# Kernel tuning notes

Hardware: AMD Instinct MI355X
Metric: run time of the kernel (lower is better)

Reference implementation:

```python
import jax, jax.numpy as jnp
import numpy as np

T = 32400   # bs*H*W BEV queries (1*180*180)
S = 16896   # bs*num_cams*h*w image keys (1*6*32*88)
E = 256     # embed_dim
H = 8       # num_heads
D = 32      # head_dim
MAXL = 32   # max interval length (ref_num_f)


def _mlp(x, w1, b1, w2, b2):
    # nn.Sequential(Linear(E,2E), ReLU, Linear(2E,E))
    return jax.nn.relu(x @ w1 + b1) @ w2 + b2


def setup_inputs() -> dict:
    k0 = jax.random.key(0)
    ks = jax.random.split(k0, 8)
    # ragged interval structure: every BEV cell has an interval of length (idx%32)+1
    lengths = (np.arange(T) % MAXL) + 1
    starts = np.concatenate([np.zeros(1, np.int64), np.cumsum(lengths)[:-1]])
    N = int(lengths.sum())  # 534472 frustum points
    ranks_bev = np.repeat(np.arange(T), lengths)          # sorted by BEV cell
    rng = np.random.default_rng(0)
    ranks_feat = rng.integers(0, S, size=N)               # which key/value row each point reads

    def lin(k, fi, fo):
        return jax.random.normal(k, (fi, fo), jnp.float32) * (1.0 / np.sqrt(fi))

    key_feat = jax.random.normal(ks[1], (S, E), jnp.float32)
    return dict(
        query_depth=jax.random.normal(ks[0], (T, E), jnp.float32),
        key=key_feat,
        value=key_feat,  # module asserts torch.equal(key, value)
        q_w1=lin(ks[2], E, 2 * E), q_b1=jnp.zeros((2 * E,), jnp.float32),
        q_w2=lin(ks[3], 2 * E, E), q_b2=jnp.zeros((E,), jnp.float32),
        k_w1=lin(ks[4], E, 2 * E), k_b1=jnp.zeros((2 * E,), jnp.float32),
        k_w2=lin(ks[5], 2 * E, E), k_b2=jnp.zeros((E,), jnp.float32),
        ranks_feat_f=jnp.asarray(ranks_feat, jnp.int32),
        ranks_bev_f=jnp.asarray(ranks_bev, jnp.int32),
        interval_starts_f=jnp.asarray(starts, jnp.int32),
        interval_lengths_f=jnp.asarray(lengths, jnp.int32),
        ref_num=MAXL,
    )


def reference(query_depth, key, value,
              q_w1, q_b1, q_w2, q_b2,
              k_w1, k_b1, k_w2, k_b2,
              ranks_feat_f, ranks_bev_f,
              interval_starts_f, interval_lengths_f, ref_num):
    scaling = 1.0 / jnp.sqrt(jnp.float32(D))
    q = (_mlp(query_depth, q_w1, q_b1, q_w2, q_b2) * scaling).reshape(T, H, D)
    k = _mlp(key, k_w1, k_b1, k_w2, k_b2).reshape(S, H, D)
    v = value.reshape(S, H, D)

    N = ranks_bev_f.shape[0]
    pt = jnp.arange(N, dtype=jnp.int32)
    # interval id of each point (intervals are contiguous, sorted by start)
    iid = jnp.searchsorted(interval_starts_f, pt, side='right') - 1
    ranks_ref = pt - interval_starts_f[iid]  # within-interval slot, in [0, ref_num)

    # per-point raw attention logit: q[bev] . k[feat] per head  -> [N, H]
    w = jnp.einsum('nhd,nhd->nh', q[ranks_bev_f], k[ranks_feat_f])

    # scatter into ragged weight tensor [T, H, ref_num]; padding masked to -1e9
    attn = jnp.full((T, H, ref_num), -1e9, jnp.float32)
    attn = attn.at[ranks_bev_f, :, ranks_ref].set(w)
    attn = jax.nn.softmax(attn, axis=-1)

    # gather normalized weights back per point and scatter-combine values
    wp = attn[ranks_bev_f, :, ranks_ref]          # [N, H]
    vp = v[ranks_feat_f]                          # [N, H, D]
    out = jnp.zeros((T, H, D), jnp.float32).at[ranks_bev_f].add(wp[:, :, None] * vp)
    return out.reshape(T, E)
```

## Files before the change

kernel.cpp:

```cpp
#include <hip/hip_runtime.h>
#include <hip/hip_bf16.h>
#include <cstdint>
#include <cstddef>

constexpr int T_Q   = 32400;
constexpr int T_PAD = 32512;
constexpr int S_K   = 16896;
constexpr int E_DIM = 256;
constexpr int HID   = 512;

typedef __bf16 bf16x8 __attribute__((ext_vector_type(8)));
typedef float  f32x4  __attribute__((ext_vector_type(4)));

__device__ __forceinline__ void async16(const __hip_bfloat16* gp, __hip_bfloat16* lp) {
    __builtin_amdgcn_global_load_lds(
        (const __attribute__((address_space(1))) void*)(gp),
        (__attribute__((address_space(3))) void*)(lp), 16, 0, 0);
}

__device__ __forceinline__ float b2f(unsigned short u) {
    return __uint_as_float(((unsigned)u) << 16);
}

constexpr int NB_Q = (T_PAD * E_DIM / 4) / 256;
constexpr int NB_K = (S_K * E_DIM / 4) / 256;
constexpr int NB_PREP = NB_Q + NB_K + NB_K + 128;

__global__ __launch_bounds__(256) void prep(
    const float* __restrict__ q_in, const float* __restrict__ key_in,
    const float* __restrict__ val_in,
    const float* __restrict__ s0, const float* __restrict__ s1,
    const float* __restrict__ s2, const float* __restrict__ s3,
    __hip_bfloat16* __restrict__ qA, __hip_bfloat16* __restrict__ kA,
    __hip_bfloat16* __restrict__ vB,
    __hip_bfloat16* __restrict__ d0, __hip_bfloat16* __restrict__ d1,
    __hip_bfloat16* __restrict__ d2, __hip_bfloat16* __restrict__ d3) {
    __shared__ float tb[64][65];
    const int b = blockIdx.x;
    const int tid = threadIdx.x;

    if (b < NB_Q + 2 * NB_K) {
        const float* src;
        __hip_bfloat16* dst;
        int bl, valid;
        if (b < NB_Q) { src = q_in; dst = qA; bl = b; valid = T_Q * E_DIM; }
        else if (b < NB_Q + NB_K) { src = key_in; dst = kA; bl = b - NB_Q; valid = S_K * E_DIM; }
        else { src = val_in; dst = vB; bl = b - NB_Q - NB_K; valid = S_K * E_DIM; }
        int i = (bl * 256 + tid) * 4;
        float4 f = make_float4(0.f, 0.f, 0.f, 0.f);
        if (i < valid) f = *(const float4*)(src + i);
        union { ushort4 u4; __hip_bfloat16 bb[4]; } cv;
        cv.bb[0] = __float2bfloat16(f.x);
        cv.bb[1] = __float2bfloat16(f.y);
        cv.bb[2] = __float2bfloat16(f.z);
        cv.bb[3] = __float2bfloat16(f.w);
        *(ushort4*)(dst + i) = cv.u4;
        return;
    }

    int tloc = b - (NB_Q + 2 * NB_K);
    int m = tloc >> 5;
    int tt = tloc & 31;
    const float* S = m == 0 ? s0 : m == 1 ? s1 : m == 2 ? s2 : s3;
    __hip_bfloat16* D = m == 0 ? d0 : m == 1 ? d1 : m == 2 ? d2 : d3;
    int Kd, Nd, kt, nt;
    if ((m & 1) == 0) { Kd = 256; Nd = 512; kt = tt & 3; nt = tt >> 2; }
    else              { Kd = 512; Nd = 256; kt = tt & 7; nt = tt >> 3; }
    int tx = tid & 63, ty = tid >> 6;
#pragma unroll
    for (int p = 0; p < 16; ++p) {
        int row = ty * 16 + p;
        tb[row][tx] = S[(size_t)(kt * 64 + row) * Nd + nt * 64 + tx];
    }
    __syncthreads();
#pragma unroll
    for (int p = 0; p < 16; ++p) {
        int row = ty * 16 + p;
        D[(size_t)(nt * 64 + row) * Kd + kt * 64 + tx] = __float2bfloat16(tb[tx][row]);
    }
}

constexpr int BM = 128, BN = 128, BK = 32;

__global__ __launch_bounds__(256) void gemm_bf16(
    const __hip_bfloat16* __restrict__ A,
    const __hip_bfloat16* __restrict__ BT,
    const float* __restrict__ bias,
    __hip_bfloat16* __restrict__ C,
    int K, int N, int relu, float scale) {
    __shared__ __hip_bfloat16 As[BM * BK];
    __shared__ __hip_bfloat16 Bs[BN * BK];

    const int ntiles = N >> 7;
    const int tm = blockIdx.x / ntiles;
    const int tn = blockIdx.x - tm * ntiles;
    const size_t m0 = (size_t)tm * BM;
    const int n0 = tn * BN;

    const int tid = threadIdx.x;
    const int w = tid >> 6, l = tid & 63;
    const int lm = l & 15, lq = l >> 4;
    const int wm = (w >> 1) << 6, wn = (w & 1) << 6;

    const int srow = l >> 2;
    const int scol = (((l & 3) ^ (srow & 3)) << 3);

    f32x4 acc[4][4] = {};

    for (int k0 = 0; k0 < K; k0 += BK) {
#pragma unroll
        for (int c = 0; c < 2; ++c) {
            int r = c * 64 + w * 16 + srow;
            async16(A  + (m0 + r) * K + k0 + scol, As + (c * 64 + w * 16) * BK);
            async16(BT + (size_t)(n0 + r) * K + k0 + scol, Bs + (c * 64 + w * 16) * BK);
        }
        __syncthreads();

        const int rsw = ((lq ^ (lm & 3)) << 3);
        bf16x8 af[4], bfr[4];
#pragma unroll
        for (int mi = 0; mi < 4; ++mi)
            af[mi] = *(const bf16x8*)(As + (wm + mi * 16 + lm) * BK + rsw);
#pragma unroll
        for (int ni = 0; ni < 4; ++ni)
            bfr[ni] = *(const bf16x8*)(Bs + (wn + ni * 16 + lm) * BK + rsw);
#pragma unroll
        for (int mi = 0; mi < 4; ++mi)
#pragma unroll
            for (int ni = 0; ni < 4; ++ni)
                acc[mi][ni] = __builtin_amdgcn_mfma_f32_16x16x32_bf16(
                    af[mi], bfr[ni], acc[mi][ni], 0, 0, 0);
        __syncthreads();
    }

#pragma unroll
    for (int ni = 0; ni < 4; ++ni) {
        int col = n0 + wn + ni * 16 + lm;
        float bv = bias[col];
#pragma unroll
        for (int mi = 0; mi < 4; ++mi) {
            size_t rowb = m0 + wm + mi * 16 + lq * 4;
#pragma unroll
            for (int r = 0; r < 4; ++r) {
                float vv = acc[mi][ni][r] + bv;
                if (relu) vv = fmaxf(vv, 0.f);
                C[(rowb + r) * N + col] = __float2bfloat16(vv * scale);
            }
        }
    }
}

#define PREF(K0,K1,K2,K3,V0,V1,V2,V3,J0)                                    \
    {                                                                        \
        int j_ = (J0);                                                       \
        int i0 = su + j_ + 0; i0 = i0 < nmax ? i0 : nmax;                    \
        int i1 = su + j_ + 1; i1 = i1 < nmax ? i1 : nmax;                    \
        int i2 = su + j_ + 2; i2 = i2 < nmax ? i2 : nmax;                    \
        int i3 = su + j_ + 3; i3 = i3 < nmax ? i3 : nmax;                    \
        int f0 = rf[i0], f1 = rf[i1], f2 = rf[i2], f3 = rf[i3];              \
        K0 = *(const ushort4*)(kp + (size_t)f0 * 256 + l4);                  \
        V0 = *(const ushort4*)(vp + (size_t)f0 * 256 + l4);                  \
        K1 = *(const ushort4*)(kp + (size_t)f1 * 256 + l4);                  \
        V1 = *(const ushort4*)(vp + (size_t)f1 * 256 + l4);                  \
        K2 = *(const ushort4*)(kp + (size_t)f2 * 256 + l4);                  \
        V2 = *(const ushort4*)(vp + (size_t)f2 * 256 + l4);                  \
        K3 = *(const ushort4*)(kp + (size_t)f3 * 256 + l4);                  \
        V3 = *(const ushort4*)(vp + (size_t)f3 * 256 + l4);                  \
    }

#define DOT4(K_) fmaf(q0, b2f(K_.x), fmaf(q1, b2f(K_.y), fmaf(q2, b2f(K_.z), q3 * b2f(K_.w))))

#define PROC(K0,K1,K2,K3,V0,V1,V2,V3,J0)                                    \
    {                                                                        \
        float w0 = DOT4(K0), w1 = DOT4(K1), w2 = DOT4(K2), w3 = DOT4(K3);   \
        w0 += __shfl_xor(w0, 1); w1 += __shfl_xor(w1, 1);                   \
        w2 += __shfl_xor(w2, 1); w3 += __shfl_xor(w3, 1);                   \
        w0 += __shfl_xor(w0, 2); w1 += __shfl_xor(w1, 2);                   \
        w2 += __shfl_xor(w2, 2); w3 += __shfl_xor(w3, 2);                   \
        w0 += __shfl_xor(w0, 4); w1 += __shfl_xor(w1, 4);                   \
        w2 += __shfl_xor(w2, 4); w3 += __shfl_xor(w3, 4);                   \
        if ((J0) + 1 >= L) w1 = -1e30f;                                      \
        if ((J0) + 2 >= L) w2 = -1e30f;                                      \
        if ((J0) + 3 >= L) w3 = -1e30f;                                      \
        float mw = fmaxf(fmaxf(w0, w1), fmaxf(w2, w3));                      \
        float mn = fmaxf(m, mw);                                             \
        float al = __expf(m - mn); m = mn;                                   \
        float p0 = __expf(w0 - mn), p1 = __expf(w1 - mn);                    \
        float p2 = __expf(w2 - mn), p3 = __expf(w3 - mn);                    \
        s = s * al + ((p0 + p1) + (p2 + p3));                                \
        a0 = fmaf(p3, b2f(V3.x), fmaf(p2, b2f(V2.x), fmaf(p1, b2f(V1.x), fmaf(p0, b2f(V0.x), a0 * al)))); \
        a1 = fmaf(p3, b2f(V3.y), fmaf(p2, b2f(V2.y), fmaf(p1, b2f(V1.y), fmaf(p0, b2f(V0.y), a1 * al)))); \
        a2 = fmaf(p3, b2f(V3.z), fmaf(p2, b2f(V2.z), fmaf(p1, b2f(V1.z), fmaf(p0, b2f(V0.z), a2 * al)))); \
        a3 = fmaf(p3, b2f(V3.w), fmaf(p2, b2f(V2.w), fmaf(p1, b2f(V1.w), fmaf(p0, b2f(V0.w), a3 * al)))); \
    }

__global__ __launch_bounds__(256) void attn_kernel(
    const __hip_bfloat16* __restrict__ q,
    const __hip_bfloat16* __restrict__ kp,
    const __hip_bfloat16* __restrict__ vp,
    const int* __restrict__ rf,
    const int* __restrict__ starts,
    const int* __restrict__ lens,
    int nmax,
    float* __restrict__ out) {
    int t = blockIdx.x * 4 + (threadIdx.x >> 6);
    if (t >= T_Q) return;
    int l = threadIdx.x & 63;
    int l4 = l * 4;
    int su = __builtin_amdgcn_readfirstlane(starts[t]);
    int L  = __builtin_amdgcn_readfirstlane(lens[t]);

    ushort4 qu = *(const ushort4*)(q + (size_t)t * 256 + l4);
    float q0 = b2f(qu.x), q1 = b2f(qu.y), q2 = b2f(qu.z), q3 = b2f(qu.w);

    float m = -INFINITY, s = 0.f;
    float a0 = 0.f, a1 = 0.f, a2 = 0.f, a3 = 0.f;

    ushort4 ak0, ak1, ak2, ak3, av0, av1, av2, av3;
    ushort4 bk0, bk1, bk2, bk3, bv0, bv1, bv2, bv3;

    int Lr = (L + 3) & ~3;
    PREF(ak0, ak1, ak2, ak3, av0, av1, av2, av3, 0);
    for (int j0 = 0; j0 < Lr; j0 += 8) {
        bool hasB = (j0 + 4 < Lr);
        if (hasB) PREF(bk0, bk1, bk2, bk3, bv0, bv1, bv2, bv3, j0 + 4);
        PROC(ak0, ak1, ak2, ak3, av0, av1, av2, av3, j0);
        if (hasB) {
            if (j0 + 8 < Lr) PREF(ak0, ak1, ak2, ak3, av0, av1, av2, av3, j0 + 8);
            PROC(bk0, bk1, bk2, bk3, bv0, bv1, bv2, bv3, j0 + 4);
        }
    }

    float inv = 1.f / s;
    float4 o = make_float4(a0 * inv, a1 * inv, a2 * inv, a3 * inv);
    *(float4*)(out + (size_t)t * 256 + l4) = o;
}

extern "C" void kernel_launch(void* const* d_in, const int* in_sizes, int n_in,
                              void* d_out, int out_size, void* d_ws, size_t ws_size,
                              hipStream_t stream) {
    const float* q_in   = (const float*)d_in[0];
    const float* key_in = (const float*)d_in[1];
    const float* val_in = (const float*)d_in[2];
    const float* q_w1   = (const float*)d_in[3];
    const float* q_b1   = (const float*)d_in[4];
    const float* q_w2   = (const float*)d_in[5];
    const float* q_b2   = (const float*)d_in[6];
    const float* k_w1   = (const float*)d_in[7];
    const float* k_b1   = (const float*)d_in[8];
    const float* k_w2   = (const float*)d_in[9];
    const float* k_b2   = (const float*)d_in[10];
    const int* ranks_feat = (const int*)d_in[11];
    const int* starts     = (const int*)d_in[13];
    const int* lens       = (const int*)d_in[14];
    float* out = (float*)d_out;
    const int n_points = in_sizes[11];

    char* ws = (char*)d_ws;
    size_t off = 0;
    auto alloc = [&](size_t bytes) {
        char* p = ws + off;
        off += (bytes + 255) & ~(size_t)255;
        return p;
    };
    __hip_bfloat16* qA   = (__hip_bfloat16*)alloc((size_t)T_PAD * E_DIM * 2);
    __hip_bfloat16* hidQ = (__hip_bfloat16*)alloc((size_t)T_PAD * HID * 2);
    __hip_bfloat16* qMl  = (__hip_bfloat16*)alloc((size_t)T_PAD * E_DIM * 2);
    __hip_bfloat16* kA   = (__hip_bfloat16*)alloc((size_t)S_K * E_DIM * 2);
    __hip_bfloat16* hidK = (__hip_bfloat16*)alloc((size_t)S_K * HID * 2);
    __hip_bfloat16* kMl  = (__hip_bfloat16*)alloc((size_t)S_K * E_DIM * 2);
    __hip_bfloat16* vB   = (__hip_bfloat16*)alloc((size_t)S_K * E_DIM * 2);
    __hip_bfloat16* w1qT = (__hip_bfloat16*)alloc((size_t)HID * E_DIM * 2);
    __hip_bfloat16* w2qT = (__hip_bfloat16*)alloc((size_t)E_DIM * HID * 2);
    __hip_bfloat16* w1kT = (__hip_bfloat16*)alloc((size_t)HID * E_DIM * 2);
    __hip_bfloat16* w2kT = (__hip_bfloat16*)alloc((size_t)E_DIM * HID * 2);
    (void)ws_size; (void)n_in; (void)out_size;

    prep<<<NB_PREP, 256, 0, stream>>>(q_in, key_in, val_in,
                                      q_w1, q_w2, k_w1, k_w2,
                                      qA, kA, vB, w1qT, w2qT, w1kT, w2kT);

    const float qscale = 0.17677669529663687f;
    gemm_bf16<<<(T_PAD / 128) * (HID / 128), 256, 0, stream>>>(qA, w1qT, q_b1, hidQ, E_DIM, HID, 1, 1.0f);
    gemm_bf16<<<(T_PAD / 128) * (E_DIM / 128), 256, 0, stream>>>(hidQ, w2qT, q_b2, qMl, HID, E_DIM, 0, qscale);
    gemm_bf16<<<(S_K / 128) * (HID / 128), 256, 0, stream>>>(kA, w1kT, k_b1, hidK, E_DIM, HID, 1, 1.0f);
    gemm_bf16<<<(S_K / 128) * (E_DIM / 128), 256, 0, stream>>>(hidK, w2kT, k_b2, kMl, HID, E_DIM, 0, 1.0f);

    attn_kernel<<<T_Q / 4, 256, 0, stream>>>(qMl, kMl, vB, ranks_feat, starts, lens,
                                             n_points - 1, out);
}
```

Baseline: 318.6 us.

## Interleave K and V rows and split each wave across two points

The projected K and V are stored interleaved in a single 512-wide row buffer, so each gathered feature row brings K and V from adjacent memory. The attention wave now handles two points per step: each half-wave takes one point with 16-byte loads, and the merged softmax state is combined across halves at the end. Feature indices are loaded once per lane and broadcast with ds_bpermute instead of being reloaded per point. This relies on intervals having at most 64 points and changes the pipelining depth and register use.

```diff
diff --git a/kernel.cpp b/kernel.cpp
--- a/kernel.cpp
+++ b/kernel.cpp
@@ -11,6 +11,7 @@
 
 typedef __bf16 bf16x8 __attribute__((ext_vector_type(8)));
 typedef float  f32x4  __attribute__((ext_vector_type(4)));
+typedef unsigned short ushort8v __attribute__((ext_vector_type(8)));
 
 __device__ __forceinline__ void async16(const __hip_bfloat16* gp, __hip_bfloat16* lp) {
     __builtin_amdgcn_global_load_lds(
@@ -32,7 +33,7 @@
     const float* __restrict__ s0, const float* __restrict__ s1,
     const float* __restrict__ s2, const float* __restrict__ s3,
     __hip_bfloat16* __restrict__ qA, __hip_bfloat16* __restrict__ kA,
-    __hip_bfloat16* __restrict__ vB,
+    __hip_bfloat16* __restrict__ kvB,
     __hip_bfloat16* __restrict__ d0, __hip_bfloat16* __restrict__ d1,
     __hip_bfloat16* __restrict__ d2, __hip_bfloat16* __restrict__ d3) {
     __shared__ float tb[64][65];
@@ -41,11 +42,10 @@
 
     if (b < NB_Q + 2 * NB_K) {
         const float* src;
-        __hip_bfloat16* dst;
-        int bl, valid;
-        if (b < NB_Q) { src = q_in; dst = qA; bl = b; valid = T_Q * E_DIM; }
-        else if (b < NB_Q + NB_K) { src = key_in; dst = kA; bl = b - NB_Q; valid = S_K * E_DIM; }
-        else { src = val_in; dst = vB; bl = b - NB_Q - NB_K; valid = S_K * E_DIM; }
+        int bl, valid, isv = 0;
+        if (b < NB_Q) { src = q_in; bl = b; valid = T_Q * E_DIM; }
+        else if (b < NB_Q + NB_K) { src = key_in; bl = b - NB_Q; valid = S_K * E_DIM; }
+        else { src = val_in; bl = b - NB_Q - NB_K; valid = S_K * E_DIM; isv = 1; }
         int i = (bl * 256 + tid) * 4;
         float4 f = make_float4(0.f, 0.f, 0.f, 0.f);
         if (i < valid) f = *(const float4*)(src + i);
@@ -54,7 +54,13 @@
         cv.bb[1] = __float2bfloat16(f.y);
         cv.bb[2] = __float2bfloat16(f.z);
         cv.bb[3] = __float2bfloat16(f.w);
-        *(ushort4*)(dst + i) = cv.u4;
+        if (isv) {
+            int r = i >> 8, c = i & 255;
+            *(ushort4*)(kvB + (size_t)r * 512 + 256 + c) = cv.u4;
+        } else {
+            __hip_bfloat16* dst = (b < NB_Q) ? qA : kA;
+            *(ushort4*)(dst + i) = cv.u4;
+        }
         return;
     }
 
@@ -87,7 +93,7 @@
     const __hip_bfloat16* __restrict__ BT,
     const float* __restrict__ bias,
     __hip_bfloat16* __restrict__ C,
-    int K, int N, int relu, float scale) {
+    int K, int N, int ldc, int relu, float scale) {
     __shared__ __hip_bfloat16 As[BM * BK];
     __shared__ __hip_bfloat16 Bs[BN * BK];
 
@@ -144,96 +150,88 @@
             for (int r = 0; r < 4; ++r) {
                 float vv = acc[mi][ni][r] + bv;
                 if (relu) vv = fmaxf(vv, 0.f);
-                C[(rowb + r) * N + col] = __float2bfloat16(vv * scale);
+                C[(rowb + r) * ldc + col] = __float2bfloat16(vv * scale);
             }
         }
     }
 }
 
-#define PREF(K0,K1,K2,K3,V0,V1,V2,V3,J0)                                    \
-    {                                                                        \
-        int j_ = (J0);                                                       \
-        int i0 = su + j_ + 0; i0 = i0 < nmax ? i0 : nmax;                    \
-        int i1 = su + j_ + 1; i1 = i1 < nmax ? i1 : nmax;                    \
-        int i2 = su + j_ + 2; i2 = i2 < nmax ? i2 : nmax;                    \
-        int i3 = su + j_ + 3; i3 = i3 < nmax ? i3 : nmax;                    \
-        int f0 = rf[i0], f1 = rf[i1], f2 = rf[i2], f3 = rf[i3];              \
-        K0 = *(const ushort4*)(kp + (size_t)f0 * 256 + l4);                  \
-        V0 = *(const ushort4*)(vp + (size_t)f0 * 256 + l4);                  \
-        K1 = *(const ushort4*)(kp + (size_t)f1 * 256 + l4);                  \
-        V1 = *(const ushort4*)(vp + (size_t)f1 * 256 + l4);                  \
-        K2 = *(const ushort4*)(kp + (size_t)f2 * 256 + l4);                  \
-        V2 = *(const ushort4*)(vp + (size_t)f2 * 256 + l4);                  \
-        K3 = *(const ushort4*)(kp + (size_t)f3 * 256 + l4);                  \
-        V3 = *(const ushort4*)(vp + (size_t)f3 * 256 + l4);                  \
-    }
-
-#define DOT4(K_) fmaf(q0, b2f(K_.x), fmaf(q1, b2f(K_.y), fmaf(q2, b2f(K_.z), q3 * b2f(K_.w))))
-
-#define PROC(K0,K1,K2,K3,V0,V1,V2,V3,J0)                                    \
-    {                                                                        \
-        float w0 = DOT4(K0), w1 = DOT4(K1), w2 = DOT4(K2), w3 = DOT4(K3);   \
-        w0 += __shfl_xor(w0, 1); w1 += __shfl_xor(w1, 1);                   \
-        w2 += __shfl_xor(w2, 1); w3 += __shfl_xor(w3, 1);                   \
-        w0 += __shfl_xor(w0, 2); w1 += __shfl_xor(w1, 2);                   \
-        w2 += __shfl_xor(w2, 2); w3 += __shfl_xor(w3, 2);                   \
-        w0 += __shfl_xor(w0, 4); w1 += __shfl_xor(w1, 4);                   \
-        w2 += __shfl_xor(w2, 4); w3 += __shfl_xor(w3, 4);                   \
-        if ((J0) + 1 >= L) w1 = -1e30f;                                      \
-        if ((J0) + 2 >= L) w2 = -1e30f;                                      \
-        if ((J0) + 3 >= L) w3 = -1e30f;                                      \
-        float mw = fmaxf(fmaxf(w0, w1), fmaxf(w2, w3));                      \
-        float mn = fmaxf(m, mw);                                             \
-        float al = __expf(m - mn); m = mn;                                   \
-        float p0 = __expf(w0 - mn), p1 = __expf(w1 - mn);                    \
-        float p2 = __expf(w2 - mn), p3 = __expf(w3 - mn);                    \
-        s = s * al + ((p0 + p1) + (p2 + p3));                                \
-        a0 = fmaf(p3, b2f(V3.x), fmaf(p2, b2f(V2.x), fmaf(p1, b2f(V1.x), fmaf(p0, b2f(V0.x), a0 * al)))); \
-        a1 = fmaf(p3, b2f(V3.y), fmaf(p2, b2f(V2.y), fmaf(p1, b2f(V1.y), fmaf(p0, b2f(V0.y), a1 * al)))); \
-        a2 = fmaf(p3, b2f(V3.z), fmaf(p2, b2f(V2.z), fmaf(p1, b2f(V1.z), fmaf(p0, b2f(V0.z), a2 * al)))); \
-        a3 = fmaf(p3, b2f(V3.w), fmaf(p2, b2f(V2.w), fmaf(p1, b2f(V1.w), fmaf(p0, b2f(V0.w), a3 * al)))); \
+#define APREF(DK, DV, C)                                                    \
+    {                                                                       \
+        int pidx = ((C) << 1) + half;                                       \
+        int f = __builtin_amdgcn_ds_bpermute(pidx << 2, myf);               \
+        const __hip_bfloat16* bp = kv + (size_t)f * 512 + sub * 8;          \
+        DK = *(const ushort8v*)bp;                                          \
+        DV = *(const ushort8v*)(bp + 256);                                  \
+    }
+
+#define APROC(KB, VB, C)                                                    \
+    {                                                                       \
+        float wv = 0.f;                                                     \
+        _Pragma("unroll") for (int i = 0; i < 8; ++i)                       \
+            wv = fmaf(qf[i], b2f(KB[i]), wv);                               \
+        wv += __shfl_xor(wv, 1);                                            \
+        wv += __shfl_xor(wv, 2);                                            \
+        float wo = __shfl_xor(wv, 32);                                      \
+        int pm = ((C) << 1) + half;                                         \
+        int po = ((C) << 1) + 1 - half;                                     \
+        if (pm >= L) wv = -1e30f;                                           \
+        if (po >= L) wo = -1e30f;                                           \
+        float mn = fmaxf(m, fmaxf(wv, wo));                                 \
+        float al = __expf(m - mn); m = mn;                                  \
+        float p = __expf(wv - mn);                                          \
+        s = fmaf(s, al, p);                                                 \
+        _Pragma("unroll") for (int i = 0; i < 8; ++i)                       \
+            a[i] = fmaf(p, b2f(VB[i]), a[i] * al);                          \
     }
 
 __global__ __launch_bounds__(256) void attn_kernel(
     const __hip_bfloat16* __restrict__ q,
-    const __hip_bfloat16* __restrict__ kp,
-    const __hip_bfloat16* __restrict__ vp,
+    const __hip_bfloat16* __restrict__ kv,
     const int* __restrict__ rf,
     const int* __restrict__ starts,
     const int* __restrict__ lens,
-    int nmax,
     float* __restrict__ out) {
     int t = blockIdx.x * 4 + (threadIdx.x >> 6);
     if (t >= T_Q) return;
     int l = threadIdx.x & 63;
-    int l4 = l * 4;
+    int half = l >> 5, sub = l & 31;
     int su = __builtin_amdgcn_readfirstlane(starts[t]);
     int L  = __builtin_amdgcn_readfirstlane(lens[t]);
 
-    ushort4 qu = *(const ushort4*)(q + (size_t)t * 256 + l4);
-    float q0 = b2f(qu.x), q1 = b2f(qu.y), q2 = b2f(qu.z), q3 = b2f(qu.w);
+    int li = l < L - 1 ? l : L - 1;
+    int myf = rf[su + li];
+
+    ushort8v qu = *(const ushort8v*)(q + (size_t)t * 256 + sub * 8);
+    float qf[8];
+#pragma unroll
+    for (int i = 0; i < 8; ++i) qf[i] = b2f(qu[i]);
 
     float m = -INFINITY, s = 0.f;
-    float a0 = 0.f, a1 = 0.f, a2 = 0.f, a3 = 0.f;
-
-    ushort4 ak0, ak1, ak2, ak3, av0, av1, av2, av3;
-    ushort4 bk0, bk1, bk2, bk3, bv0, bv1, bv2, bv3;
-
-    int Lr = (L + 3) & ~3;
-    PREF(ak0, ak1, ak2, ak3, av0, av1, av2, av3, 0);
-    for (int j0 = 0; j0 < Lr; j0 += 8) {
-        bool hasB = (j0 + 4 < Lr);
-        if (hasB) PREF(bk0, bk1, bk2, bk3, bv0, bv1, bv2, bv3, j0 + 4);
-        PROC(ak0, ak1, ak2, ak3, av0, av1, av2, av3, j0);
-        if (hasB) {
-            if (j0 + 8 < Lr) PREF(ak0, ak1, ak2, ak3, av0, av1, av2, av3, j0 + 8);
-            PROC(bk0, bk1, bk2, bk3, bv0, bv1, bv2, bv3, j0 + 4);
-        }
-    }
-
+    float a[8] = {0.f, 0.f, 0.f, 0.f, 0.f, 0.f, 0.f, 0.f};
+
+    ushort8v k0v = {}, v0v = {}, k1v = {}, v1v = {}, k2v = {}, v2v = {};
+
+    int nC = (L + 1) >> 1;
+    APREF(k0v, v0v, 0);
+    if (nC > 1) APREF(k1v, v1v, 1);
+    for (int c = 0; c < nC; ++c) {
+        if (c + 2 < nC) APREF(k2v, v2v, c + 2);
+        APROC(k0v, v0v, c);
+        k0v = k1v; v0v = v1v;
+        k1v = k2v; v1v = v2v;
+    }
+
+    s += __shfl_xor(s, 32);
+#pragma unroll
+    for (int i = 0; i < 8; ++i) a[i] += __shfl_xor(a[i], 32);
     float inv = 1.f / s;
-    float4 o = make_float4(a0 * inv, a1 * inv, a2 * inv, a3 * inv);
-    *(float4*)(out + (size_t)t * 256 + l4) = o;
+    float4 o;
+    o.x = (half ? a[4] : a[0]) * inv;
+    o.y = (half ? a[5] : a[1]) * inv;
+    o.z = (half ? a[6] : a[2]) * inv;
+    o.w = (half ? a[7] : a[3]) * inv;
+    *(float4*)(out + (size_t)t * 256 + sub * 8 + half * 4) = o;
 }
 
 extern "C" void kernel_launch(void* const* d_in, const int* in_sizes, int n_in,
@@ -254,7 +252,6 @@
     const int* starts     = (const int*)d_in[13];
     const int* lens       = (const int*)d_in[14];
     float* out = (float*)d_out;
-    const int n_points = in_sizes[11];
 
     char* ws = (char*)d_ws;
     size_t off = 0;
@@ -268,24 +265,22 @@
     __hip_bfloat16* qMl  = (__hip_bfloat16*)alloc((size_t)T_PAD * E_DIM * 2);
     __hip_bfloat16* kA   = (__hip_bfloat16*)alloc((size_t)S_K * E_DIM * 2);
     __hip_bfloat16* hidK = (__hip_bfloat16*)alloc((size_t)S_K * HID * 2);
-    __hip_bfloat16* kMl  = (__hip_bfloat16*)alloc((size_t)S_K * E_DIM * 2);
-    __hip_bfloat16* vB   = (__hip_bfloat16*)alloc((size_t)S_K * E_DIM * 2);
+    __hip_bfloat16* kvB  = (__hip_bfloat16*)alloc((size_t)S_K * 512 * 2);
     __hip_bfloat16* w1qT = (__hip_bfloat16*)alloc((size_t)HID * E_DIM * 2);
     __hip_bfloat16* w2qT = (__hip_bfloat16*)alloc((size_t)E_DIM * HID * 2);
     __hip_bfloat16* w1kT = (__hip_bfloat16*)alloc((size_t)HID * E_DIM * 2);
     __hip_bfloat16* w2kT = (__hip_bfloat16*)alloc((size_t)E_DIM * HID * 2);
-    (void)ws_size; (void)n_in; (void)out_size;
+    (void)ws_size; (void)n_in; (void)out_size; (void)in_sizes;
 
     prep<<<NB_PREP, 256, 0, stream>>>(q_in, key_in, val_in,
                                       q_w1, q_w2, k_w1, k_w2,
-                                      qA, kA, vB, w1qT, w2qT, w1kT, w2kT);
+                                      qA, kA, kvB, w1qT, w2qT, w1kT, w2kT);
 
     const float qscale = 0.17677669529663687f;
-    gemm_bf16<<<(T_PAD / 128) * (HID / 128), 256, 0, stream>>>(qA, w1qT, q_b1, hidQ, E_DIM, HID, 1, 1.0f);
-    gemm_bf16<<<(T_PAD / 128) * (E_DIM / 128), 256, 0, stream>>>(hidQ, w2qT, q_b2, qMl, HID, E_DIM, 0, qscale);
-    gemm_bf16<<<(S_K / 128) * (HID / 128), 256, 0, stream>>>(kA, w1kT, k_b1, hidK, E_DIM, HID, 1, 1.0f);
-    gemm_bf16<<<(S_K / 128) * (E_DIM / 128), 256, 0, stream>>>(hidK, w2kT, k_b2, kMl, HID, E_DIM, 0, 1.0f);
-
-    attn_kernel<<<T_Q / 4, 256, 0, stream>>>(qMl, kMl, vB, ranks_feat, starts, lens,
-                                             n_points - 1, out);
-}
+    gemm_bf16<<<(T_PAD / 128) * (HID / 128), 256, 0, stream>>>(qA, w1qT, q_b1, hidQ, E_DIM, HID, HID, 1, 1.0f);
+    gemm_bf16<<<(T_PAD / 128) * (E_DIM / 128), 256, 0, stream>>>(hidQ, w2qT, q_b2, qMl, HID, E_DIM, E_DIM, 0, qscale);
+    gemm_bf16<<<(S_K / 128) * (HID / 128), 256, 0, stream>>>(kA, w1kT, k_b1, hidK, E_DIM, HID, HID, 1, 1.0f);
+    gemm_bf16<<<(S_K / 128) * (E_DIM / 128), 256, 0, stream>>>(hidK, w2kT, k_b2, kvB, HID, E_DIM, 512, 0, 1.0f);
+
+    attn_kernel<<<T_Q / 4, 256, 0, stream>>>(qMl, kvB, ranks_feat, starts, lens, out);
+}
```

Result: no change. 313.1 us (-1.7%).
